# Performance work log

Measured on AMD Instinct MI355X. Metric: run time of the kernel, lower is better.

## Reference

```python
import jax, jax.numpy as jnp
import numpy as np

B = 128
K = 16
# (in_ch, featdim, dim) per stage, matching conv1..conv11
DIMS = [(3, 8, 2048), (8, 32, 1024), (32, 64, 512), (64, 64, 256), (64, 64, 128),
        (64, 128, 64), (128, 256, 32), (256, 512, 16), (512, 512, 8), (512, 512, 4),
        (512, 1024, 2)]


def setup_inputs() -> dict:
    key = jax.random.key(0)
    ks = jax.random.split(key, 64)
    inp = {"x": jax.random.normal(ks[0], (B, 3, 2048), dtype=jnp.float32)}
    i = 1
    for li, (cin, cf, d) in enumerate(DIMS, start=1):
        inp[f"W{li}"] = jax.random.normal(ks[i], (3 * cf, cin), dtype=jnp.float32) / np.sqrt(cin).astype(np.float32); i += 1
        inp[f"b{li}"] = jax.random.normal(ks[i], (3 * cf,), dtype=jnp.float32) * 0.01; i += 1
        inp[f"sel{li}"] = jax.random.randint(ks[i], (d,), 0, 3); i += 1
    inp["fcW"] = jax.random.normal(ks[i], (K, 1024), dtype=jnp.float32) / np.sqrt(1024).astype(np.float32); i += 1
    inp["fcb"] = jax.random.normal(ks[i], (K,), dtype=jnp.float32) * 0.01
    return inp


def kdconv(x, W, b, sel, featdim, dim):
    # 1x1 conv == per-position matmul: x [B, Cin, dim] -> y [B, 3*featdim, dim]
    y = jax.nn.relu(jnp.einsum('oi,bin->bon', W, x) + b[None, :, None])
    y = y.reshape(-1, featdim, 3, dim)
    # kd split-dim gather: pick one of the 3 feature groups per position
    y = jnp.take_along_axis(y, sel[None, None, None, :], axis=2)[:, :, 0, :]  # [B, featdim, dim]
    # pairwise max-pool of sibling leaves
    return y.reshape(-1, featdim, dim // 2, 2).max(axis=-1)  # [B, featdim, dim//2]


def reference(x, sel1, sel2, sel3, sel4, sel5, sel6, sel7, sel8, sel9, sel10, sel11,
              W1, b1, W2, b2, W3, b3, W4, b4, W5, b5, W6, b6, W7, b7, W8, b8,
              W9, b9, W10, b10, W11, b11, fcW, fcb):
    Ws = [W1, W2, W3, W4, W5, W6, W7, W8, W9, W10, W11]
    bs = [b1, b2, b3, b4, b5, b6, b7, b8, b9, b10, b11]
    sels = [sel1, sel2, sel3, sel4, sel5, sel6, sel7, sel8, sel9, sel10, sel11]
    h = x
    for (cin, cf, d), W, b, s in zip(DIMS, Ws, bs, sels):
        h = kdconv(h, W, b, s, cf, d)
    h = h.reshape(-1, 1024)  # [B, 1024]
    return jax.nn.log_softmax(h @ fcW.T + fcb, axis=-1)
```

## Files before the change

### kernel.cpp

```cpp
#include <hip/hip_runtime.h>
#include <math.h>

typedef __attribute__((ext_vector_type(8))) short bf16x8;
typedef __attribute__((ext_vector_type(4))) float f32x4;

__device__ __forceinline__ unsigned short f2bf(float f) {
    unsigned u = __builtin_bit_cast(unsigned, f);
    u += 0x7FFF + ((u >> 16) & 1);
    return (unsigned short)(u >> 16);
}
__device__ __forceinline__ float bf2f(unsigned short h) {
    unsigned u = ((unsigned)h) << 16;
    return __builtin_bit_cast(float, u);
}

struct K1Params {
    const float* x;
    const float* W1; const float* B1; const int* S1;
    const float* W2; const float* B2; const int* S2;
    const float* Wsrc[9];
    unsigned short* Wb;
    unsigned short* X3;
};

__global__ __launch_bounds__(256) void k1_kernel(K1Params P)
{
    const int tid = threadIdx.x;

    if (blockIdx.x >= 128) {
        int gt = (blockIdx.x - 128) * 256 + tid;
        const int we[9] = {6144, 12288, 12288, 24576, 98304, 393216, 786432, 786432, 1572864};
        int off = 0;
#pragma unroll
        for (int li = 0; li < 9; ++li) {
            const float4* src = (const float4*)P.Wsrc[li];
            ushort4* dst = (ushort4*)(P.Wb + off);
            int n4 = we[li] >> 2;
            for (int i = gt; i < n4; i += 32768) {
                float4 w = src[i];
                dst[i] = make_ushort4(f2bf(w.x), f2bf(w.y), f2bf(w.z), f2bf(w.w));
            }
            off += we[li];
        }
        return;
    }

    __shared__ float wl1[72], bl1[24], wl2[768], bl2[96];
    __shared__ unsigned short bufL1[16 * 64 * 8];

    if (tid < 72) wl1[tid] = P.W1[tid];
    if (tid >= 128 && tid < 152) bl1[tid - 128] = P.B1[tid - 128];
    for (int i = tid; i < 768; i += 256) wl2[i] = P.W2[i];
    if (tid < 96) bl2[tid] = P.B2[tid];
    __syncthreads();

    const int npT = blockIdx.x >> 1;
    const int b0  = (blockIdx.x & 1) * 64;

    for (int i = tid; i < 1024; i += 256) {
        int pos_l = i >> 6, bl = i & 63;
        int np1 = npT * 16 + pos_l;
        int b = b0 + bl;
        int s0 = P.S1[2 * np1], s1 = P.S1[2 * np1 + 1];
        const float* xb = P.x + (size_t)b * 6144 + 2 * np1;
        float2 c0 = *(const float2*)(xb);
        float2 c1 = *(const float2*)(xb + 2048);
        float2 c2 = *(const float2*)(xb + 4096);
        unsigned short o[8];
#pragma unroll
        for (int f = 0; f < 8; ++f) {
            int r0 = f * 3 + s0, r1 = f * 3 + s1;
            float z0 = fmaf(wl1[r0*3+2], c2.x, fmaf(wl1[r0*3+1], c1.x, fmaf(wl1[r0*3+0], c0.x, bl1[r0])));
            float z1 = fmaf(wl1[r1*3+2], c2.y, fmaf(wl1[r1*3+1], c1.y, fmaf(wl1[r1*3+0], c0.y, bl1[r1])));
            o[f] = f2bf(fmaxf(fmaxf(z0, z1), 0.f));
        }
        unsigned short* dst = &bufL1[((size_t)pos_l * 64 + bl) * 8];
        *(ushort4*)dst       = make_ushort4(o[0], o[1], o[2], o[3]);
        *(ushort4*)(dst + 4) = make_ushort4(o[4], o[5], o[6], o[7]);
    }
    __syncthreads();

    for (int i = tid; i < 512; i += 256) {
        int np_l = i >> 6, bl = i & 63;
        int np2 = npT * 8 + np_l;
        int s0 = P.S2[2 * np2], s1 = P.S2[2 * np2 + 1];
        const unsigned short* r0 = &bufL1[((size_t)(2 * np_l) * 64 + bl) * 8];
        const unsigned short* r1 = &bufL1[((size_t)(2 * np_l + 1) * 64 + bl) * 8];
        float xa[8], xb[8];
        {
            ushort4 u0 = *(const ushort4*)r0, u1 = *(const ushort4*)(r0 + 4);
            ushort4 v0 = *(const ushort4*)r1, v1 = *(const ushort4*)(r1 + 4);
            xa[0]=bf2f(u0.x); xa[1]=bf2f(u0.y); xa[2]=bf2f(u0.z); xa[3]=bf2f(u0.w);
            xa[4]=bf2f(u1.x); xa[5]=bf2f(u1.y); xa[6]=bf2f(u1.z); xa[7]=bf2f(u1.w);
            xb[0]=bf2f(v0.x); xb[1]=bf2f(v0.y); xb[2]=bf2f(v0.z); xb[3]=bf2f(v0.w);
            xb[4]=bf2f(v1.x); xb[5]=bf2f(v1.y); xb[6]=bf2f(v1.z); xb[7]=bf2f(v1.w);
        }
        unsigned short o[32];
#pragma unroll
        for (int f = 0; f < 32; ++f) {
            const float* w0 = &wl2[(f * 3 + s0) * 8];
            const float* w1 = &wl2[(f * 3 + s1) * 8];
            float z0 = bl2[f * 3 + s0], z1 = bl2[f * 3 + s1];
#pragma unroll
            for (int k = 0; k < 8; ++k) {
                z0 = fmaf(w0[k], xa[k], z0);
                z1 = fmaf(w1[k], xb[k], z1);
            }
            o[f] = f2bf(fmaxf(fmaxf(z0, z1), 0.f));
        }
        unsigned short* dst = P.X3 + ((size_t)np2 * 128 + b0 + bl) * 32;
#pragma unroll
        for (int i2 = 0; i2 < 8; ++i2)
            *(ushort4*)(dst + 4 * i2) = make_ushort4(o[4*i2], o[4*i2+1], o[4*i2+2], o[4*i2+3]);
    }
}

template<int CIN>
__device__ __forceinline__ void mfma_tile(
    const unsigned short* a0, const unsigned short* a1,
    const unsigned short* b0p, const unsigned short* b1p,
    f32x4& acc0, f32x4& acc1)
{
#pragma unroll
    for (int k = 0; k < CIN; k += 32) {
        bf16x8 A0 = __builtin_bit_cast(bf16x8, *(const float4*)(const void*)(a0 + k));
        bf16x8 A1 = __builtin_bit_cast(bf16x8, *(const float4*)(const void*)(a1 + k));
        bf16x8 B0 = __builtin_bit_cast(bf16x8, *(const float4*)(const void*)(b0p + k));
        bf16x8 B1 = __builtin_bit_cast(bf16x8, *(const float4*)(const void*)(b1p + k));
        acc0 = __builtin_amdgcn_mfma_f32_16x16x32_bf16(A0, B0, acc0, 0, 0, 0);
        acc1 = __builtin_amdgcn_mfma_f32_16x16x32_bf16(A1, B1, acc1, 0, 0, 0);
    }
}

__device__ __forceinline__ void epilogue_store(
    unsigned short* dst, const f32x4& acc0, const f32x4& acc1,
    const float* bias, int fbase, int s0, int s1)
{
    unsigned short o[4];
#pragma unroll
    for (int r = 0; r < 4; ++r) {
        float v = fmaxf(fmaxf(acc0[r] + bias[(fbase + r) * 3 + s0],
                              acc1[r] + bias[(fbase + r) * 3 + s1]), 0.f);
        o[r] = f2bf(v);
    }
    *(ushort4*)dst = make_ushort4(o[0], o[1], o[2], o[3]);
}

__global__ __launch_bounds__(256) void stage2_kernel(
    const unsigned short* __restrict__ X3,
    const unsigned short* __restrict__ Wb,
    const float* __restrict__ B3, const int* __restrict__ S3,
    const float* __restrict__ B4, const int* __restrict__ S4,
    const float* __restrict__ B5, const int* __restrict__ S5,
    unsigned short* __restrict__ X6)
{
    constexpr int RPE = 72;
    __shared__ unsigned short L3o[4 * 32 * RPE];
    __shared__ unsigned short L4o[2 * 32 * RPE];

    const int tid  = threadIdx.x;
    const int lane = tid & 63;
    const int wv   = tid >> 6;
    const int c = lane & 15, q = lane >> 4;
    const int n5 = blockIdx.x >> 2;
    const int b0 = (blockIdx.x & 3) * 32;

    const unsigned short* W3b = Wb;
    const unsigned short* W4b = Wb + 6144;
    const unsigned short* W5b = Wb + 18432;

    for (int t = wv; t < 32; t += 4) {
        int bt = t & 1, ft = (t >> 1) & 3, j = t >> 3;
        int np = 4 * n5 + j;
        int s0 = __builtin_amdgcn_readfirstlane(S3[2 * np]);
        int s1 = __builtin_amdgcn_readfirstlane(S3[2 * np + 1]);
        int f0 = ft * 16, bl = bt * 16;
        const unsigned short* a0 = W3b + (size_t)((f0 + c) * 3 + s0) * 32 + q * 8;
        const unsigned short* a1 = W3b + (size_t)((f0 + c) * 3 + s1) * 32 + q * 8;
        const unsigned short* bp0 = X3 + ((size_t)(8 * n5 + 2 * j) * 128 + b0 + bl + c) * 32 + q * 8;
        const unsigned short* bp1 = X3 + ((size_t)(8 * n5 + 2 * j + 1) * 128 + b0 + bl + c) * 32 + q * 8;
        f32x4 acc0 = {0.f,0.f,0.f,0.f}, acc1 = {0.f,0.f,0.f,0.f};
        mfma_tile<32>(a0, a1, bp0, bp1, acc0, acc1);
        epilogue_store(&L3o[((size_t)j * 32 + bl + c) * RPE + f0 + q * 4],
                       acc0, acc1, B3, f0 + q * 4, s0, s1);
    }
    __syncthreads();

    for (int t = wv; t < 16; t += 4) {
        int bt = t & 1, ft = (t >> 1) & 3, j = t >> 3;
        int np = 2 * n5 + j;
        int s0 = __builtin_amdgcn_readfirstlane(S4[2 * np]);
        int s1 = __builtin_amdgcn_readfirstlane(S4[2 * np + 1]);
        int f0 = ft * 16, bl = bt * 16;
        const unsigned short* a0 = W4b + (size_t)((f0 + c) * 3 + s0) * 64 + q * 8;
        const unsigned short* a1 = W4b + (size_t)((f0 + c) * 3 + s1) * 64 + q * 8;
        const unsigned short* bp0 = &L3o[((size_t)(2 * j) * 32 + bl + c) * RPE + q * 8];
        const unsigned short* bp1 = &L3o[((size_t)(2 * j + 1) * 32 + bl + c) * RPE + q * 8];
        f32x4 acc0 = {0.f,0.f,0.f,0.f}, acc1 = {0.f,0.f,0.f,0.f};
        mfma_tile<64>(a0, a1, bp0, bp1, acc0, acc1);
        epilogue_store(&L4o[((size_t)j * 32 + bl + c) * RPE + f0 + q * 4],
                       acc0, acc1, B4, f0 + q * 4, s0, s1);
    }
    __syncthreads();

    for (int t = wv; t < 8; t += 4) {
        int bt = t & 1, ft = t >> 1;
        int s0 = __builtin_amdgcn_readfirstlane(S5[2 * n5]);
        int s1 = __builtin_amdgcn_readfirstlane(S5[2 * n5 + 1]);
        int f0 = ft * 16, bl = bt * 16;
        const unsigned short* a0 = W5b + (size_t)((f0 + c) * 3 + s0) * 64 + q * 8;
        const unsigned short* a1 = W5b + (size_t)((f0 + c) * 3 + s1) * 64 + q * 8;
        const unsigned short* bp0 = &L4o[((size_t)(0) * 32 + bl + c) * RPE + q * 8];
        const unsigned short* bp1 = &L4o[((size_t)(1) * 32 + bl + c) * RPE + q * 8];
        f32x4 acc0 = {0.f,0.f,0.f,0.f}, acc1 = {0.f,0.f,0.f,0.f};
        mfma_tile<64>(a0, a1, bp0, bp1, acc0, acc1);
        epilogue_store(X6 + ((size_t)n5 * 128 + b0 + bl + c) * 64 + f0 + q * 4,
                       acc0, acc1, B5, f0 + q * 4, s0, s1);
    }
}

__global__ __launch_bounds__(512) void stage67_kernel(
    const unsigned short* __restrict__ X6,
    const unsigned short* __restrict__ W6b, const float* __restrict__ B6, const int* __restrict__ S6,
    const unsigned short* __restrict__ W7b, const float* __restrict__ B7, const int* __restrict__ S7,
    unsigned short* __restrict__ X8)
{
    constexpr int RPE = 136;
    __shared__ unsigned short L6o[2 * 16 * RPE];

    const int tid  = threadIdx.x;
    const int lane = tid & 63;
    const int wv   = tid >> 6;
    const int c = lane & 15, q = lane >> 4;
    const int n7 = blockIdx.x >> 3;
    const int b0 = (blockIdx.x & 7) * 16;

    for (int t = wv; t < 16; t += 8) {
        int j = t >> 3, ft = t & 7;
        int np = 2 * n7 + j;
        int s0 = __builtin_amdgcn_readfirstlane(S6[2 * np]);
        int s1 = __builtin_amdgcn_readfirstlane(S6[2 * np + 1]);
        int f0 = ft * 16;
        const unsigned short* a0 = W6b + (size_t)((f0 + c) * 3 + s0) * 64 + q * 8;
        const unsigned short* a1 = W6b + (size_t)((f0 + c) * 3 + s1) * 64 + q * 8;
        const unsigned short* bp0 = X6 + ((size_t)(2 * np) * 128 + b0 + c) * 64 + q * 8;
        const unsigned short* bp1 = X6 + ((size_t)(2 * np + 1) * 128 + b0 + c) * 64 + q * 8;
        f32x4 acc0 = {0.f,0.f,0.f,0.f}, acc1 = {0.f,0.f,0.f,0.f};
        mfma_tile<64>(a0, a1, bp0, bp1, acc0, acc1);
        epilogue_store(&L6o[((size_t)j * 16 + c) * RPE + f0 + q * 4],
                       acc0, acc1, B6, f0 + q * 4, s0, s1);
    }
    __syncthreads();

    {
        int s0 = __builtin_amdgcn_readfirstlane(S7[2 * n7]);
        int s1 = __builtin_amdgcn_readfirstlane(S7[2 * n7 + 1]);
        for (int t = wv; t < 16; t += 8) {
            int f0 = t * 16;
            const unsigned short* a0 = W7b + (size_t)((f0 + c) * 3 + s0) * 128 + q * 8;
            const unsigned short* a1 = W7b + (size_t)((f0 + c) * 3 + s1) * 128 + q * 8;
            const unsigned short* bp0 = &L6o[((size_t)(0) * 16 + c) * RPE + q * 8];
            const unsigned short* bp1 = &L6o[((size_t)(1) * 16 + c) * RPE + q * 8];
            f32x4 acc0 = {0.f,0.f,0.f,0.f}, acc1 = {0.f,0.f,0.f,0.f};
            mfma_tile<128>(a0, a1, bp0, bp1, acc0, acc1);
            epilogue_store(X8 + ((size_t)n7 * 128 + b0 + c) * 256 + f0 + q * 4,
                           acc0, acc1, B7, f0 + q * 4, s0, s1);
        }
    }
}

template<int CIN, int CF, int NP, int MW, int NW>
__global__ __launch_bounds__(256) void mfma_kernel(
    const unsigned short* __restrict__ Xin,
    const unsigned short* __restrict__ Wb,
    const float* __restrict__ bias,
    const int*   __restrict__ sel,
    unsigned short* __restrict__ Xout)
{
    constexpr int FT = CF / (16 * MW);
    constexpr int BT = 128 / (16 * NW);

    const int wid  = threadIdx.x >> 6;
    const int lane = threadIdx.x & 63;
    const int task = blockIdx.x * 4 + wid;
    const int bi = task % BT;
    const int fi = (task / BT) % FT;
    const int n  = task / (BT * FT);

    const int c = lane & 15;
    const int q = lane >> 4;
    const int s0 = __builtin_amdgcn_readfirstlane(sel[2 * n]);
    const int s1 = __builtin_amdgcn_readfirstlane(sel[2 * n + 1]);

    const int f0 = fi * 16 * MW;
    const int b0 = bi * 16 * NW;

    const unsigned short* ap[2][MW];
    const unsigned short* bp[2][NW];
#pragma unroll
    for (int p = 0; p < 2; ++p) {
        int s = p ? s1 : s0;
#pragma unroll
        for (int mi = 0; mi < MW; ++mi)
            ap[p][mi] = Wb + (size_t)((f0 + mi * 16 + c) * 3 + s) * CIN + q * 8;
#pragma unroll
        for (int ni = 0; ni < NW; ++ni)
            bp[p][ni] = Xin + ((size_t)(2 * n + p) * 128 + b0 + ni * 16 + c) * CIN + q * 8;
    }

    f32x4 acc[2][MW][NW];
#pragma unroll
    for (int p = 0; p < 2; ++p)
#pragma unroll
        for (int mi = 0; mi < MW; ++mi)
#pragma unroll
            for (int ni = 0; ni < NW; ++ni)
                acc[p][mi][ni] = (f32x4){0.f, 0.f, 0.f, 0.f};

// ... 33 lines not shown

__global__ __launch_bounds__(256) void fc_logsoftmax_kernel(
    const unsigned short* __restrict__ h, const float* __restrict__ fcW,
    const float* __restrict__ fcb, float* __restrict__ out)
{
    int b   = blockIdx.x;
    int tid = threadIdx.x;
    int k     = tid & 15;
    int chunk = tid >> 4;

    const float* __restrict__ wk = fcW + (size_t)k * 1024;
    const unsigned short* hb = h + (size_t)b * 1024;

    float partial = 0.0f;
    int j0 = chunk * 64;
#pragma unroll 8
    for (int j = 0; j < 64; ++j)
        partial = fmaf(bf2f(hb[j0 + j]), wk[j0 + j], partial);

    __shared__ float red[16][17];
    red[chunk][k] = partial;
    __syncthreads();

    __shared__ float logits[16];
    if (tid < 16) {
        float s = fcb[tid];
#pragma unroll
        for (int c = 0; c < 16; ++c) s += red[c][tid];
        logits[tid] = s;
    }
    __syncthreads();

    if (tid < 16) {
        float mx = -INFINITY;
#pragma unroll
        for (int kk = 0; kk < 16; ++kk) mx = fmaxf(mx, logits[kk]);
        float se = 0.0f;
#pragma unroll
        for (int kk = 0; kk < 16; ++kk) se += expf(logits[kk] - mx);
        out[b * 16 + tid] = logits[tid] - mx - logf(se);
    }
}

extern "C" void kernel_launch(void* const* d_in, const int* in_sizes, int n_in,
                              void* d_out, int out_size, void* d_ws, size_t ws_size,
                              hipStream_t stream)
{
#define WL(i) (const float*)d_in[1 + 3 * (i)]
#define BL(i) (const float*)d_in[2 + 3 * (i)]
#define SL(i) (const int*)  d_in[3 + 3 * (i)]

    unsigned short* bufA = (unsigned short*)d_ws;
    unsigned short* bufB = bufA + 2u * 1024u * 1024u;
    unsigned short* Wb   = bufB + 2u * 1024u * 1024u;

    const int o6 = 30720, o7 = 55296, o8 = 153600,
              o9 = 546816, o10 = 1333248, o11 = 2119680;

    K1Params P;
    P.x = (const float*)d_in[0];
    P.W1 = WL(0); P.B1 = BL(0); P.S1 = SL(0);
    P.W2 = WL(1); P.B2 = BL(1); P.S2 = SL(1);
    for (int i = 0; i < 9; ++i) P.Wsrc[i] = WL(2 + i);
    P.Wb = Wb; P.X3 = bufA;
    k1_kernel<<<256, 256, 0, stream>>>(P);

    stage2_kernel<<<256, 256, 0, stream>>>(bufA, Wb,
        BL(2), SL(2), BL(3), SL(3), BL(4), SL(4), bufB);

    stage67_kernel<<<128, 512, 0, stream>>>(bufB,
        Wb + o6, BL(5), SL(5), Wb + o7, BL(6), SL(6), bufA);

    mfma_kernel<256, 512, 8, 2, 2><<<128, 256, 0, stream>>>(bufA, Wb + o8,  BL(7),  SL(7),  bufB);
    mfma_kernel<512, 512, 4, 1, 1><<<256, 256, 0, stream>>>(bufB, Wb + o9,  BL(8),  SL(8),  bufA);
    mfma_kernel<512, 512, 2, 1, 1><<<128, 256, 0, stream>>>(bufA, Wb + o10, BL(9),  SL(9),  bufB);
    mfma_kernel<512, 1024, 1, 1, 1><<<128, 256, 0, stream>>>(bufB, Wb + o11, BL(10), SL(10), bufA);

    fc_logsoftmax_kernel<<<128, 256, 0, stream>>>(bufA, (const float*)d_in[34], (const float*)d_in[35], (float*)d_out);

#undef WL
#undef BL
#undef SL
}
```

Before: 211.0 us.

## Fuse stages 1-7 into one kernel with per-block tree slices in LDS

Replaces the three kernels for layers 1-7 with one fused kernel. Each block owns 16 batch items and one 128-point slice of the tree and keeps every intermediate level in a reused shared-memory arena, so activations no longer make round trips through global memory and two launches go away. Each block converts the weights for layers 3-6 from fp32 to bf16 into LDS, and layer 7 converts its weights on the fly, while extra blocks convert only the layer 8-11 weights. The cost is redundant weight conversion in every block, a large LDS footprint that limits occupancy, and fewer parallel tiles per level.

```diff
diff --git a/kernel.cpp b/kernel.cpp
--- a/kernel.cpp
+++ b/kernel.cpp
@@ -14,106 +14,10 @@
     return __builtin_bit_cast(float, u);
 }
 
-struct K1Params {
-    const float* x;
-    const float* W1; const float* B1; const int* S1;
-    const float* W2; const float* B2; const int* S2;
-    const float* Wsrc[9];
-    unsigned short* Wb;
-    unsigned short* X3;
-};
-
-__global__ __launch_bounds__(256) void k1_kernel(K1Params P)
-{
-    const int tid = threadIdx.x;
-
-    if (blockIdx.x >= 128) {
-        int gt = (blockIdx.x - 128) * 256 + tid;
-        const int we[9] = {6144, 12288, 12288, 24576, 98304, 393216, 786432, 786432, 1572864};
-        int off = 0;
-#pragma unroll
-        for (int li = 0; li < 9; ++li) {
-            const float4* src = (const float4*)P.Wsrc[li];
-            ushort4* dst = (ushort4*)(P.Wb + off);
-            int n4 = we[li] >> 2;
-            for (int i = gt; i < n4; i += 32768) {
-                float4 w = src[i];
-                dst[i] = make_ushort4(f2bf(w.x), f2bf(w.y), f2bf(w.z), f2bf(w.w));
-            }
-            off += we[li];
-        }
-        return;
-    }
-
-    __shared__ float wl1[72], bl1[24], wl2[768], bl2[96];
-    __shared__ unsigned short bufL1[16 * 64 * 8];
-
-    if (tid < 72) wl1[tid] = P.W1[tid];
-    if (tid >= 128 && tid < 152) bl1[tid - 128] = P.B1[tid - 128];
-    for (int i = tid; i < 768; i += 256) wl2[i] = P.W2[i];
-    if (tid < 96) bl2[tid] = P.B2[tid];
-    __syncthreads();
-
-    const int npT = blockIdx.x >> 1;
-    const int b0  = (blockIdx.x & 1) * 64;
-
-    for (int i = tid; i < 1024; i += 256) {
-        int pos_l = i >> 6, bl = i & 63;
-        int np1 = npT * 16 + pos_l;
-        int b = b0 + bl;
-        int s0 = P.S1[2 * np1], s1 = P.S1[2 * np1 + 1];
-        const float* xb = P.x + (size_t)b * 6144 + 2 * np1;
-        float2 c0 = *(const float2*)(xb);
-        float2 c1 = *(const float2*)(xb + 2048);
-        float2 c2 = *(const float2*)(xb + 4096);
-        unsigned short o[8];
-#pragma unroll
-        for (int f = 0; f < 8; ++f) {
-            int r0 = f * 3 + s0, r1 = f * 3 + s1;
-            float z0 = fmaf(wl1[r0*3+2], c2.x, fmaf(wl1[r0*3+1], c1.x, fmaf(wl1[r0*3+0], c0.x, bl1[r0])));
-            float z1 = fmaf(wl1[r1*3+2], c2.y, fmaf(wl1[r1*3+1], c1.y, fmaf(wl1[r1*3+0], c0.y, bl1[r1])));
-            o[f] = f2bf(fmaxf(fmaxf(z0, z1), 0.f));
-        }
-        unsigned short* dst = &bufL1[((size_t)pos_l * 64 + bl) * 8];
-        *(ushort4*)dst       = make_ushort4(o[0], o[1], o[2], o[3]);
-        *(ushort4*)(dst + 4) = make_ushort4(o[4], o[5], o[6], o[7]);
-    }
-    __syncthreads();
-
-    for (int i = tid; i < 512; i += 256) {
-        int np_l = i >> 6, bl = i & 63;
-        int np2 = npT * 8 + np_l;
-        int s0 = P.S2[2 * np2], s1 = P.S2[2 * np2 + 1];
-        const unsigned short* r0 = &bufL1[((size_t)(2 * np_l) * 64 + bl) * 8];
-        const unsigned short* r1 = &bufL1[((size_t)(2 * np_l + 1) * 64 + bl) * 8];
-        float xa[8], xb[8];
-        {
-            ushort4 u0 = *(const ushort4*)r0, u1 = *(const ushort4*)(r0 + 4);
-            ushort4 v0 = *(const ushort4*)r1, v1 = *(const ushort4*)(r1 + 4);
-            xa[0]=bf2f(u0.x); xa[1]=bf2f(u0.y); xa[2]=bf2f(u0.z); xa[3]=bf2f(u0.w);
-            xa[4]=bf2f(u1.x); xa[5]=bf2f(u1.y); xa[6]=bf2f(u1.z); xa[7]=bf2f(u1.w);
-            xb[0]=bf2f(v0.x); xb[1]=bf2f(v0.y); xb[2]=bf2f(v0.z); xb[3]=bf2f(v0.w);
-            xb[4]=bf2f(v1.x); xb[5]=bf2f(v1.y); xb[6]=bf2f(v1.z); xb[7]=bf2f(v1.w);
-        }
-        unsigned short o[32];
-#pragma unroll
-        for (int f = 0; f < 32; ++f) {
-            const float* w0 = &wl2[(f * 3 + s0) * 8];
-            const float* w1 = &wl2[(f * 3 + s1) * 8];
-            float z0 = bl2[f * 3 + s0], z1 = bl2[f * 3 + s1];
-#pragma unroll
-            for (int k = 0; k < 8; ++k) {
-                z0 = fmaf(w0[k], xa[k], z0);
-                z1 = fmaf(w1[k], xb[k], z1);
-            }
-            o[f] = f2bf(fmaxf(fmaxf(z0, z1), 0.f));
-        }
-        unsigned short* dst = P.X3 + ((size_t)np2 * 128 + b0 + bl) * 32;
-#pragma unroll
-        for (int i2 = 0; i2 < 8; ++i2)
-            *(ushort4*)(dst + 4 * i2) = make_ushort4(o[4*i2], o[4*i2+1], o[4*i2+2], o[4*i2+3]);
-    }
-}
+#define O_W8 153600
+#define O_W9 546816
+#define O_W10 1333248
+#define O_W11 2119680
 
 template<int CIN>
 __device__ __forceinline__ void mfma_tile(
@@ -146,124 +50,317 @@
     *(ushort4*)dst = make_ushort4(o[0], o[1], o[2], o[3]);
 }
 
-__global__ __launch_bounds__(256) void stage2_kernel(
-    const unsigned short* __restrict__ X3,
-    const unsigned short* __restrict__ Wb,
-    const float* __restrict__ B3, const int* __restrict__ S3,
-    const float* __restrict__ B4, const int* __restrict__ S4,
-    const float* __restrict__ B5, const int* __restrict__ S5,
-    unsigned short* __restrict__ X6)
+__device__ __forceinline__ bf16x8 cvt8(const float* p) {
+    float4 u0 = *(const float4*)p;
+    float4 u1 = *(const float4*)(p + 4);
+    bf16x8 r;
+    r[0] = (short)f2bf(u0.x); r[1] = (short)f2bf(u0.y);
+    r[2] = (short)f2bf(u0.z); r[3] = (short)f2bf(u0.w);
+    r[4] = (short)f2bf(u1.x); r[5] = (short)f2bf(u1.y);
+    r[6] = (short)f2bf(u1.z); r[7] = (short)f2bf(u1.w);
+    return r;
+}
+
+struct FusedParams {
+    const float* x;
+    const float* W1; const float* B1; const int* S1;
+    const float* W2; const float* B2; const int* S2;
+    const float* Wsrc[9];
+    const float* Bl[9];
+    const int*   Sl[9];
+    unsigned short* Wb;
+    unsigned short* X8;
+};
+
+#define A_XS   0
+#define A_L1O  25344
+#define A_WSM  41728
+#define A_L2O  45568
+#define A_WB3  0
+#define A_L3O  86528
+#define A_WB4  45568
+#define A_L4O  0
+#define A_WB5  18432
+#define A_L5O  46080
+#define A_WB6  55296
+#define A_L6O  0
+#define ARENA_BYTES 123392
+
+__global__ __launch_bounds__(512) void fused17_kernel(FusedParams P)
 {
-    constexpr int RPE = 72;
-    __shared__ unsigned short L3o[4 * 32 * RPE];
-    __shared__ unsigned short L4o[2 * 32 * RPE];
-
-    const int tid  = threadIdx.x;
+    const int tid = threadIdx.x;
+
+    if (blockIdx.x >= 128) {
+        int gt = (blockIdx.x - 128) * 512 + tid;
+        const int we[4] = {393216, 786432, 786432, 1572864};
+        const int wo[4] = {O_W8, O_W9, O_W10, O_W11};
+#pragma unroll
+        for (int li = 0; li < 4; ++li) {
+            const float4* src = (const float4*)P.Wsrc[5 + li];
+            ushort4* dst = (ushort4*)(P.Wb + wo[li]);
+            int n4 = we[li] >> 2;
+            for (int i = gt; i < n4; i += 32768) {
+                float4 w = src[i];
+                dst[i] = make_ushort4(f2bf(w.x), f2bf(w.y), f2bf(w.z), f2bf(w.w));
+            }
+        }
+        return;
+    }
+
+    __shared__ __align__(16) char arena[ARENA_BYTES];
+
+    const int bg   = blockIdx.x >> 4;
+    const int sl   = blockIdx.x & 15;
     const int lane = tid & 63;
     const int wv   = tid >> 6;
-    const int c = lane & 15, q = lane >> 4;
-    const int n5 = blockIdx.x >> 2;
-    const int b0 = (blockIdx.x & 3) * 32;
-
-    const unsigned short* W3b = Wb;
-    const unsigned short* W4b = Wb + 6144;
-    const unsigned short* W5b = Wb + 18432;
-
-    for (int t = wv; t < 32; t += 4) {
-        int bt = t & 1, ft = (t >> 1) & 3, j = t >> 3;
-        int np = 4 * n5 + j;
-        int s0 = __builtin_amdgcn_readfirstlane(S3[2 * np]);
-        int s1 = __builtin_amdgcn_readfirstlane(S3[2 * np + 1]);
-        int f0 = ft * 16, bl = bt * 16;
-        const unsigned short* a0 = W3b + (size_t)((f0 + c) * 3 + s0) * 32 + q * 8;
-        const unsigned short* a1 = W3b + (size_t)((f0 + c) * 3 + s1) * 32 + q * 8;
-        const unsigned short* bp0 = X3 + ((size_t)(8 * n5 + 2 * j) * 128 + b0 + bl + c) * 32 + q * 8;
-        const unsigned short* bp1 = X3 + ((size_t)(8 * n5 + 2 * j + 1) * 128 + b0 + bl + c) * 32 + q * 8;
-        f32x4 acc0 = {0.f,0.f,0.f,0.f}, acc1 = {0.f,0.f,0.f,0.f};
-        mfma_tile<32>(a0, a1, bp0, bp1, acc0, acc1);
-        epilogue_store(&L3o[((size_t)j * 32 + bl + c) * RPE + f0 + q * 4],
-                       acc0, acc1, B3, f0 + q * 4, s0, s1);
-    }
-    __syncthreads();
-
-    for (int t = wv; t < 16; t += 4) {
-        int bt = t & 1, ft = (t >> 1) & 3, j = t >> 3;
-        int np = 2 * n5 + j;
-        int s0 = __builtin_amdgcn_readfirstlane(S4[2 * np]);
-        int s1 = __builtin_amdgcn_readfirstlane(S4[2 * np + 1]);
-        int f0 = ft * 16, bl = bt * 16;
-        const unsigned short* a0 = W4b + (size_t)((f0 + c) * 3 + s0) * 64 + q * 8;
-        const unsigned short* a1 = W4b + (size_t)((f0 + c) * 3 + s1) * 64 + q * 8;
-        const unsigned short* bp0 = &L3o[((size_t)(2 * j) * 32 + bl + c) * RPE + q * 8];
-        const unsigned short* bp1 = &L3o[((size_t)(2 * j + 1) * 32 + bl + c) * RPE + q * 8];
-        f32x4 acc0 = {0.f,0.f,0.f,0.f}, acc1 = {0.f,0.f,0.f,0.f};
-        mfma_tile<64>(a0, a1, bp0, bp1, acc0, acc1);
-        epilogue_store(&L4o[((size_t)j * 32 + bl + c) * RPE + f0 + q * 4],
-                       acc0, acc1, B4, f0 + q * 4, s0, s1);
-    }
-    __syncthreads();
-
-    for (int t = wv; t < 8; t += 4) {
-        int bt = t & 1, ft = t >> 1;
-        int s0 = __builtin_amdgcn_readfirstlane(S5[2 * n5]);
-        int s1 = __builtin_amdgcn_readfirstlane(S5[2 * n5 + 1]);
-        int f0 = ft * 16, bl = bt * 16;
-        const unsigned short* a0 = W5b + (size_t)((f0 + c) * 3 + s0) * 64 + q * 8;
-        const unsigned short* a1 = W5b + (size_t)((f0 + c) * 3 + s1) * 64 + q * 8;
-        const unsigned short* bp0 = &L4o[((size_t)(0) * 32 + bl + c) * RPE + q * 8];
-        const unsigned short* bp1 = &L4o[((size_t)(1) * 32 + bl + c) * RPE + q * 8];
-        f32x4 acc0 = {0.f,0.f,0.f,0.f}, acc1 = {0.f,0.f,0.f,0.f};
-        mfma_tile<64>(a0, a1, bp0, bp1, acc0, acc1);
-        epilogue_store(X6 + ((size_t)n5 * 128 + b0 + bl + c) * 64 + f0 + q * 4,
-                       acc0, acc1, B5, f0 + q * 4, s0, s1);
-    }
-}
-
-__global__ __launch_bounds__(512) void stage67_kernel(
-    const unsigned short* __restrict__ X6,
-    const unsigned short* __restrict__ W6b, const float* __restrict__ B6, const int* __restrict__ S6,
-    const unsigned short* __restrict__ W7b, const float* __restrict__ B7, const int* __restrict__ S7,
-    unsigned short* __restrict__ X8)
-{
-    constexpr int RPE = 136;
-    __shared__ unsigned short L6o[2 * 16 * RPE];
-
-    const int tid  = threadIdx.x;
-    const int lane = tid & 63;
-    const int wv   = tid >> 6;
-    const int c = lane & 15, q = lane >> 4;
-    const int n7 = blockIdx.x >> 3;
-    const int b0 = (blockIdx.x & 7) * 16;
-
-    for (int t = wv; t < 16; t += 8) {
-        int j = t >> 3, ft = t & 7;
-        int np = 2 * n7 + j;
-        int s0 = __builtin_amdgcn_readfirstlane(S6[2 * np]);
-        int s1 = __builtin_amdgcn_readfirstlane(S6[2 * np + 1]);
-        int f0 = ft * 16;
-        const unsigned short* a0 = W6b + (size_t)((f0 + c) * 3 + s0) * 64 + q * 8;
-        const unsigned short* a1 = W6b + (size_t)((f0 + c) * 3 + s1) * 64 + q * 8;
-        const unsigned short* bp0 = X6 + ((size_t)(2 * np) * 128 + b0 + c) * 64 + q * 8;
-        const unsigned short* bp1 = X6 + ((size_t)(2 * np + 1) * 128 + b0 + c) * 64 + q * 8;
-        f32x4 acc0 = {0.f,0.f,0.f,0.f}, acc1 = {0.f,0.f,0.f,0.f};
-        mfma_tile<64>(a0, a1, bp0, bp1, acc0, acc1);
-        epilogue_store(&L6o[((size_t)j * 16 + c) * RPE + f0 + q * 4],
-                       acc0, acc1, B6, f0 + q * 4, s0, s1);
-    }
-    __syncthreads();
-
-    {
-        int s0 = __builtin_amdgcn_readfirstlane(S7[2 * n7]);
-        int s1 = __builtin_amdgcn_readfirstlane(S7[2 * n7 + 1]);
+    const int c    = lane & 15, q = lane >> 4;
+
+    {
+        float* xsf = (float*)(arena + A_XS);
+        const float* xg = P.x + (size_t)(bg * 16) * 6144 + sl * 128;
+        for (int i = tid; i < 6144; i += 512) {
+            int b = i / 384;
+            int r = i - b * 384;
+            int cc = r >> 7, p = r & 127;
+            xsf[b * 396 + cc * 132 + p] = xg[(size_t)b * 6144 + cc * 2048 + p];
+        }
+        float* wsm = (float*)(arena + A_WSM);
+        for (int i = tid; i < 960; i += 512) {
+            float v;
+            if (i < 72)       v = P.W1[i];
+            else if (i < 96)  v = P.B1[i - 72];
+            else if (i < 864) v = P.W2[i - 96];
+            else              v = P.B2[i - 864];
+            wsm[i] = v;
+        }
+    }
+    __syncthreads();
+
+    {
+        const float* xsf = (const float*)(arena + A_XS);
+        const float* wl1 = (const float*)(arena + A_WSM);
+        const float* bl1 = wl1 + 72;
+        unsigned short* L1o = (unsigned short*)(arena + A_L1O);
+        for (int i = tid; i < 1024; i += 512) {
+            int n = i >> 4, b = i & 15;
+            int np1 = sl * 64 + n;
+            int s0 = P.S1[2 * np1], s1 = P.S1[2 * np1 + 1];
+            const float* xb0 = xsf + b * 396 + 2 * n;
+            float c0x = xb0[0],   c0y = xb0[1];
+            float c1x = xb0[132], c1y = xb0[133];
+            float c2x = xb0[264], c2y = xb0[265];
+            unsigned short o[8];
+#pragma unroll
+            for (int f = 0; f < 8; ++f) {
+                int r0 = f * 3 + s0, r1 = f * 3 + s1;
+                float z0 = fmaf(wl1[r0*3+2], c2x, fmaf(wl1[r0*3+1], c1x, fmaf(wl1[r0*3+0], c0x, bl1[r0])));
+                float z1 = fmaf(wl1[r1*3+2], c2y, fmaf(wl1[r1*3+1], c1y, fmaf(wl1[r1*3+0], c0y, bl1[r1])));
+                o[f] = f2bf(fmaxf(fmaxf(z0, z1), 0.f));
+            }
+            unsigned short* dst = L1o + (n * 16 + b) * 8;
+            *(ushort4*)dst       = make_ushort4(o[0], o[1], o[2], o[3]);
+            *(ushort4*)(dst + 4) = make_ushort4(o[4], o[5], o[6], o[7]);
+        }
+    }
+    __syncthreads();
+
+    {
+        const float* wl2 = (const float*)(arena + A_WSM) + 96;
+        const float* bl2 = (const float*)(arena + A_WSM) + 864;
+        const unsigned short* L1o = (const unsigned short*)(arena + A_L1O);
+        unsigned short* L2o = (unsigned short*)(arena + A_L2O);
+        {
+            int i = tid;
+            int n = i >> 4, b = i & 15;
+            int np2 = sl * 32 + n;
+            int s0 = P.S2[2 * np2], s1 = P.S2[2 * np2 + 1];
+            const unsigned short* r0 = L1o + ((2 * n) * 16 + b) * 8;
+            const unsigned short* r1 = L1o + ((2 * n + 1) * 16 + b) * 8;
+            float xa[8], xb2[8];
+            {
+                ushort4 u0 = *(const ushort4*)r0, u1 = *(const ushort4*)(r0 + 4);
+                ushort4 v0 = *(const ushort4*)r1, v1 = *(const ushort4*)(r1 + 4);
+                xa[0]=bf2f(u0.x); xa[1]=bf2f(u0.y); xa[2]=bf2f(u0.z); xa[3]=bf2f(u0.w);
+                xa[4]=bf2f(u1.x); xa[5]=bf2f(u1.y); xa[6]=bf2f(u1.z); xa[7]=bf2f(u1.w);
+                xb2[0]=bf2f(v0.x); xb2[1]=bf2f(v0.y); xb2[2]=bf2f(v0.z); xb2[3]=bf2f(v0.w);
+                xb2[4]=bf2f(v1.x); xb2[5]=bf2f(v1.y); xb2[6]=bf2f(v1.z); xb2[7]=bf2f(v1.w);
+            }
+            unsigned short o[32];
+#pragma unroll
+            for (int f = 0; f < 32; ++f) {
+                const float* w0 = &wl2[(f * 3 + s0) * 8];
+                const float* w1 = &wl2[(f * 3 + s1) * 8];
+                float z0 = bl2[f * 3 + s0], z1 = bl2[f * 3 + s1];
+#pragma unroll
+                for (int k = 0; k < 8; ++k) {
+                    z0 = fmaf(w0[k], xa[k], z0);
+                    z1 = fmaf(w1[k], xb2[k], z1);
+                }
+                o[f] = f2bf(fmaxf(fmaxf(z0, z1), 0.f));
+            }
+            unsigned short* dst = L2o + (n * 16 + b) * 40;
+#pragma unroll
+            for (int i2 = 0; i2 < 8; ++i2)
+                *(ushort4*)(dst + 4 * i2) = make_ushort4(o[4*i2], o[4*i2+1], o[4*i2+2], o[4*i2+3]);
+        }
+    }
+    __syncthreads();
+
+    {
+        unsigned short* wb = (unsigned short*)(arena + A_WB3);
+        const float* Wf = P.Wsrc[0];
+        for (int i = tid; i < 6144; i += 512) {
+            int row = i >> 5, k = i & 31;
+            wb[row * 40 + k] = f2bf(Wf[i]);
+        }
+    }
+    __syncthreads();
+
+    {
+        const unsigned short* wb  = (const unsigned short*)(arena + A_WB3);
+        const unsigned short* L2o = (const unsigned short*)(arena + A_L2O);
+        unsigned short* L3o = (unsigned short*)(arena + A_L3O);
+        const int* S3 = P.Sl[0]; const float* B3 = P.Bl[0];
+        for (int t = wv; t < 64; t += 8) {
+            int n3 = t >> 2, ft = t & 3;
+            int np = sl * 16 + n3;
+            int s0 = __builtin_amdgcn_readfirstlane(S3[2 * np]);
+            int s1 = __builtin_amdgcn_readfirstlane(S3[2 * np + 1]);
+            int f0 = ft * 16;
+            const unsigned short* a0 = wb + ((f0 + c) * 3 + s0) * 40 + q * 8;
+            const unsigned short* a1 = wb + ((f0 + c) * 3 + s1) * 40 + q * 8;
+            const unsigned short* bp0 = L2o + ((2 * n3) * 16 + c) * 40 + q * 8;
+            const unsigned short* bp1 = L2o + ((2 * n3 + 1) * 16 + c) * 40 + q * 8;
+            f32x4 acc0 = {0.f,0.f,0.f,0.f}, acc1 = {0.f,0.f,0.f,0.f};
+            mfma_tile<32>(a0, a1, bp0, bp1, acc0, acc1);
+            epilogue_store(L3o + (n3 * 16 + c) * 72 + f0 + q * 4,
+                           acc0, acc1, B3, f0 + q * 4, s0, s1);
+        }
+    }
+    __syncthreads();
+
+    {
+        unsigned short* wb = (unsigned short*)(arena + A_WB4);
+        const float* Wf = P.Wsrc[1];
+        for (int i = tid; i < 12288; i += 512) {
+            int row = i >> 6, k = i & 63;
+            wb[row * 72 + k] = f2bf(Wf[i]);
+        }
+    }
+    __syncthreads();
+
+    {
+        const unsigned short* wb  = (const unsigned short*)(arena + A_WB4);
+        const unsigned short* L3o = (const unsigned short*)(arena + A_L3O);
+        unsigned short* L4o = (unsigned short*)(arena + A_L4O);
+        const int* S4 = P.Sl[1]; const float* B4 = P.Bl[1];
+        for (int t = wv; t < 32; t += 8) {
+            int n4 = t >> 2, ft = t & 3;
+            int np = sl * 8 + n4;
+            int s0 = __builtin_amdgcn_readfirstlane(S4[2 * np]);
+            int s1 = __builtin_amdgcn_readfirstlane(S4[2 * np + 1]);
+            int f0 = ft * 16;
+            const unsigned short* a0 = wb + ((f0 + c) * 3 + s0) * 72 + q * 8;
+            const unsigned short* a1 = wb + ((f0 + c) * 3 + s1) * 72 + q * 8;
+            const unsigned short* bp0 = L3o + ((2 * n4) * 16 + c) * 72 + q * 8;
+            const unsigned short* bp1 = L3o + ((2 * n4 + 1) * 16 + c) * 72 + q * 8;
+            f32x4 acc0 = {0.f,0.f,0.f,0.f}, acc1 = {0.f,0.f,0.f,0.f};
+            mfma_tile<64>(a0, a1, bp0, bp1, acc0, acc1);
+            epilogue_store(L4o + (n4 * 16 + c) * 72 + f0 + q * 4,
+                           acc0, acc1, B4, f0 + q * 4, s0, s1);
+        }
+    }
+    __syncthreads();
+
+    {
+        unsigned short* wb = (unsigned short*)(arena + A_WB5);
+        const float* Wf = P.Wsrc[2];
+        for (int i = tid; i < 12288; i += 512) {
+            int row = i >> 6, k = i & 63;
+            wb[row * 72 + k] = f2bf(Wf[i]);
+        }
+    }
+    __syncthreads();
+
+    {
+        const unsigned short* wb  = (const unsigned short*)(arena + A_WB5);
+        const unsigned short* L4o = (const unsigned short*)(arena + A_L4O);
+        unsigned short* L5o = (unsigned short*)(arena + A_L5O);
+        const int* S5 = P.Sl[2]; const float* B5 = P.Bl[2];
+        for (int t = wv; t < 16; t += 8) {
+            int n5 = t >> 2, ft = t & 3;
+            int np = sl * 4 + n5;
+            int s0 = __builtin_amdgcn_readfirstlane(S5[2 * np]);
+            int s1 = __builtin_amdgcn_readfirstlane(S5[2 * np + 1]);
+            int f0 = ft * 16;
+            const unsigned short* a0 = wb + ((f0 + c) * 3 + s0) * 72 + q * 8;
+            const unsigned short* a1 = wb + ((f0 + c) * 3 + s1) * 72 + q * 8;
+            const unsigned short* bp0 = L4o + ((2 * n5) * 16 + c) * 72 + q * 8;
+            const unsigned short* bp1 = L4o + ((2 * n5 + 1) * 16 + c) * 72 + q * 8;
+            f32x4 acc0 = {0.f,0.f,0.f,0.f}, acc1 = {0.f,0.f,0.f,0.f};
+            mfma_tile<64>(a0, a1, bp0, bp1, acc0, acc1);
+            epilogue_store(L5o + (n5 * 16 + c) * 72 + f0 + q * 4,
+                           acc0, acc1, B5, f0 + q * 4, s0, s1);
+        }
+    }
+    __syncthreads();
+
+    {
+        unsigned short* wb = (unsigned short*)(arena + A_WB6);
+        const float* Wf = P.Wsrc[3];
+        for (int i = tid; i < 24576; i += 512) {
+            int row = i >> 6, k = i & 63;
+            wb[row * 72 + k] = f2bf(Wf[i]);
+        }
+    }
+    __syncthreads();
+
+    {
+        const unsigned short* wb  = (const unsigned short*)(arena + A_WB6);
+        const unsigned short* L5o = (const unsigned short*)(arena + A_L5O);
+        unsigned short* L6o = (unsigned short*)(arena + A_L6O);
+        const int* S6 = P.Sl[3]; const float* B6 = P.Bl[3];
+        for (int t = wv; t < 16; t += 8) {
+            int n6 = t >> 3, ft = t & 7;
+            int np = sl * 2 + n6;
+            int s0 = __builtin_amdgcn_readfirstlane(S6[2 * np]);
+            int s1 = __builtin_amdgcn_readfirstlane(S6[2 * np + 1]);
+            int f0 = ft * 16;
+            const unsigned short* a0 = wb + ((f0 + c) * 3 + s0) * 72 + q * 8;
+            const unsigned short* a1 = wb + ((f0 + c) * 3 + s1) * 72 + q * 8;
+            const unsigned short* bp0 = L5o + ((2 * n6) * 16 + c) * 72 + q * 8;
+            const unsigned short* bp1 = L5o + ((2 * n6 + 1) * 16 + c) * 72 + q * 8;
+            f32x4 acc0 = {0.f,0.f,0.f,0.f}, acc1 = {0.f,0.f,0.f,0.f};
+            mfma_tile<64>(a0, a1, bp0, bp1, acc0, acc1);
+            epilogue_store(L6o + (n6 * 16 + c) * 136 + f0 + q * 4,
+                           acc0, acc1, B6, f0 + q * 4, s0, s1);
+        }
+    }
+    __syncthreads();
+
+    {
+        const unsigned short* L6o = (const unsigned short*)(arena + A_L6O);
+        const float* W7f = P.Wsrc[4];
+        const int* S7 = P.Sl[4]; const float* B7 = P.Bl[4];
+        int s0 = __builtin_amdgcn_readfirstlane(S7[2 * sl]);
+        int s1 = __builtin_amdgcn_readfirstlane(S7[2 * sl + 1]);
         for (int t = wv; t < 16; t += 8) {
             int f0 = t * 16;
-            const unsigned short* a0 = W7b + (size_t)((f0 + c) * 3 + s0) * 128 + q * 8;
-            const unsigned short* a1 = W7b + (size_t)((f0 + c) * 3 + s1) * 128 + q * 8;
-            const unsigned short* bp0 = &L6o[((size_t)(0) * 16 + c) * RPE + q * 8];
-            const unsigned short* bp1 = &L6o[((size_t)(1) * 16 + c) * RPE + q * 8];
+            const float* wa0 = W7f + (size_t)((f0 + c) * 3 + s0) * 128;
+            const float* wa1 = W7f + (size_t)((f0 + c) * 3 + s1) * 128;
+            const unsigned short* bp0 = L6o + (0 * 16 + c) * 136;
+            const unsigned short* bp1 = L6o + (1 * 16 + c) * 136;
             f32x4 acc0 = {0.f,0.f,0.f,0.f}, acc1 = {0.f,0.f,0.f,0.f};
-            mfma_tile<128>(a0, a1, bp0, bp1, acc0, acc1);
-            epilogue_store(X8 + ((size_t)n7 * 128 + b0 + c) * 256 + f0 + q * 4,
+#pragma unroll
+            for (int k = 0; k < 128; k += 32) {
+                bf16x8 A0 = cvt8(wa0 + k + q * 8);
+                bf16x8 A1 = cvt8(wa1 + k + q * 8);
+                bf16x8 B0 = __builtin_bit_cast(bf16x8, *(const float4*)(const void*)(bp0 + k + q * 8));
+                bf16x8 B1 = __builtin_bit_cast(bf16x8, *(const float4*)(const void*)(bp1 + k + q * 8));
+                acc0 = __builtin_amdgcn_mfma_f32_16x16x32_bf16(A0, B0, acc0, 0, 0, 0);
+                acc1 = __builtin_amdgcn_mfma_f32_16x16x32_bf16(A1, B1, acc1, 0, 0, 0);
+            }
+            epilogue_store(P.X8 + ((size_t)sl * 128 + bg * 16 + c) * 256 + f0 + q * 4,
                            acc0, acc1, B7, f0 + q * 4, s0, s1);
         }
     }
@@ -405,27 +502,22 @@
     unsigned short* bufB = bufA + 2u * 1024u * 1024u;
     unsigned short* Wb   = bufB + 2u * 1024u * 1024u;
 
-    const int o6 = 30720, o7 = 55296, o8 = 153600,
-              o9 = 546816, o10 = 1333248, o11 = 2119680;
-
-    K1Params P;
-    P.x = (const float*)d_in[0];
-    P.W1 = WL(0); P.B1 = BL(0); P.S1 = SL(0);
-    P.W2 = WL(1); P.B2 = BL(1); P.S2 = SL(1);
-    for (int i = 0; i < 9; ++i) P.Wsrc[i] = WL(2 + i);
-    P.Wb = Wb; P.X3 = bufA;
-    k1_kernel<<<256, 256, 0, stream>>>(P);
-
-    stage2_kernel<<<256, 256, 0, stream>>>(bufA, Wb,
-        BL(2), SL(2), BL(3), SL(3), BL(4), SL(4), bufB);
-
-    stage67_kernel<<<128, 512, 0, stream>>>(bufB,
-        Wb + o6, BL(5), SL(5), Wb + o7, BL(6), SL(6), bufA);
-
-    mfma_kernel<256, 512, 8, 2, 2><<<128, 256, 0, stream>>>(bufA, Wb + o8,  BL(7),  SL(7),  bufB);
-    mfma_kernel<512, 512, 4, 1, 1><<<256, 256, 0, stream>>>(bufB, Wb + o9,  BL(8),  SL(8),  bufA);
-    mfma_kernel<512, 512, 2, 1, 1><<<128, 256, 0, stream>>>(bufA, Wb + o10, BL(9),  SL(9),  bufB);
-    mfma_kernel<512, 1024, 1, 1, 1><<<128, 256, 0, stream>>>(bufB, Wb + o11, BL(10), SL(10), bufA);
+    FusedParams FP;
+    FP.x  = (const float*)d_in[0];
+    FP.W1 = WL(0); FP.B1 = BL(0); FP.S1 = SL(0);
+    FP.W2 = WL(1); FP.B2 = BL(1); FP.S2 = SL(1);
+    for (int i = 0; i < 9; ++i) {
+        FP.Wsrc[i] = WL(2 + i);
+        FP.Bl[i]   = BL(2 + i);
+        FP.Sl[i]   = SL(2 + i);
+    }
+    FP.Wb = Wb; FP.X8 = bufA;
+    fused17_kernel<<<192, 512, 0, stream>>>(FP);
+
+    mfma_kernel<256, 512, 8, 2, 2><<<128, 256, 0, stream>>>(bufA, Wb + O_W8,  BL(7),  SL(7),  bufB);
+    mfma_kernel<512, 512, 4, 1, 1><<<256, 256, 0, stream>>>(bufB, Wb + O_W9,  BL(8),  SL(8),  bufA);
+    mfma_kernel<512, 512, 2, 1, 1><<<128, 256, 0, stream>>>(bufA, Wb + O_W10, BL(9),  SL(9),  bufB);
+    mfma_kernel<512, 1024, 1, 1, 1><<<128, 256, 0, stream>>>(bufB, Wb + O_W11, BL(10), SL(10), bufA);
 
     fc_logsoftmax_kernel<<<128, 256, 0, stream>>>(bufA, (const float*)d_in[34], (const float*)d_in[35], (float*)d_out);
 
```

Result: no change. 208.7 us (-1.1%).

## Restructure head kernel to compute L1+L2 per thread without shared staging

Applied to the files above, without the earlier changes.

The first kernel now assigns each thread one level-2 output position for one batch element. It loads four input positions with float4 reads and computes layer 1 in registers, removing the shared-memory bufL1 staging and the barrier between layers 1 and 2. The grid doubles to 512 blocks, and the weight-packing blocks also double, so each converts with a larger stride. X3 moves to its own workspace buffer and weight offsets become named constants. This adds occupancy, but L2 output stores are now strided per lane (np2*128 + b), which may reduce coalescing.

```diff
diff --git a/kernel.cpp b/kernel.cpp
--- a/kernel.cpp
+++ b/kernel.cpp
@@ -14,7 +14,48 @@
     return __builtin_bit_cast(float, u);
 }
 
-struct K1Params {
+#define O_W3 0
+#define O_W4 6144
+#define O_W5 18432
+#define O_W6 30720
+#define O_W7 55296
+#define O_W8 153600
+#define O_W9 546816
+#define O_W10 1333248
+#define O_W11 2119680
+
+template<int CIN>
+__device__ __forceinline__ void mfma_tile(
+    const unsigned short* a0, const unsigned short* a1,
+    const unsigned short* b0p, const unsigned short* b1p,
+    f32x4& acc0, f32x4& acc1)
+{
+#pragma unroll
+    for (int k = 0; k < CIN; k += 32) {
+        bf16x8 A0 = __builtin_bit_cast(bf16x8, *(const float4*)(const void*)(a0 + k));
+        bf16x8 A1 = __builtin_bit_cast(bf16x8, *(const float4*)(const void*)(a1 + k));
+        bf16x8 B0 = __builtin_bit_cast(bf16x8, *(const float4*)(const void*)(b0p + k));
+        bf16x8 B1 = __builtin_bit_cast(bf16x8, *(const float4*)(const void*)(b1p + k));
+        acc0 = __builtin_amdgcn_mfma_f32_16x16x32_bf16(A0, B0, acc0, 0, 0, 0);
+        acc1 = __builtin_amdgcn_mfma_f32_16x16x32_bf16(A1, B1, acc1, 0, 0, 0);
+    }
+}
+
+__device__ __forceinline__ void epilogue_store(
+    unsigned short* dst, const f32x4& acc0, const f32x4& acc1,
+    const float* bias, int fbase, int s0, int s1)
+{
+    unsigned short o[4];
+#pragma unroll
+    for (int r = 0; r < 4; ++r) {
+        float v = fmaxf(fmaxf(acc0[r] + bias[(fbase + r) * 3 + s0],
+                              acc1[r] + bias[(fbase + r) * 3 + s1]), 0.f);
+        o[r] = f2bf(v);
+    }
+    *(ushort4*)dst = make_ushort4(o[0], o[1], o[2], o[3]);
+}
+
+struct HeadParams {
     const float* x;
     const float* W1; const float* B1; const int* S1;
     const float* W2; const float* B2; const int* S2;
@@ -23,79 +64,79 @@
     unsigned short* X3;
 };
 
-__global__ __launch_bounds__(256) void k1_kernel(K1Params P)
+__global__ __launch_bounds__(256) void head_l12_pack(HeadParams P)
 {
     const int tid = threadIdx.x;
 
-    if (blockIdx.x >= 128) {
-        int gt = (blockIdx.x - 128) * 256 + tid;
+    if (blockIdx.x >= 256) {
+        int gt = (blockIdx.x - 256) * 256 + tid;
         const int we[9] = {6144, 12288, 12288, 24576, 98304, 393216, 786432, 786432, 1572864};
-        int off = 0;
+        const int wo[9] = {O_W3, O_W4, O_W5, O_W6, O_W7, O_W8, O_W9, O_W10, O_W11};
 #pragma unroll
         for (int li = 0; li < 9; ++li) {
             const float4* src = (const float4*)P.Wsrc[li];
-            ushort4* dst = (ushort4*)(P.Wb + off);
+            ushort4* dst = (ushort4*)(P.Wb + wo[li]);
             int n4 = we[li] >> 2;
-            for (int i = gt; i < n4; i += 32768) {
+            for (int i = gt; i < n4; i += 65536) {
                 float4 w = src[i];
                 dst[i] = make_ushort4(f2bf(w.x), f2bf(w.y), f2bf(w.z), f2bf(w.w));
             }
-            off += we[li];
         }
         return;
     }
 
-    __shared__ float wl1[72], bl1[24], wl2[768], bl2[96];
-    __shared__ unsigned short bufL1[16 * 64 * 8];
-
-    if (tid < 72) wl1[tid] = P.W1[tid];
-    if (tid >= 128 && tid < 152) bl1[tid - 128] = P.B1[tid - 128];
-    for (int i = tid; i < 768; i += 256) wl2[i] = P.W2[i];
-    if (tid < 96) bl2[tid] = P.B2[tid];
-    __syncthreads();
-
-    const int npT = blockIdx.x >> 1;
-    const int b0  = (blockIdx.x & 1) * 64;
-
-    for (int i = tid; i < 1024; i += 256) {
-        int pos_l = i >> 6, bl = i & 63;
-        int np1 = npT * 16 + pos_l;
-        int b = b0 + bl;
-        int s0 = P.S1[2 * np1], s1 = P.S1[2 * np1 + 1];
-        const float* xb = P.x + (size_t)b * 6144 + 2 * np1;
-        float2 c0 = *(const float2*)(xb);
-        float2 c1 = *(const float2*)(xb + 2048);
-        float2 c2 = *(const float2*)(xb + 4096);
-        unsigned short o[8];
+    __shared__ float wsm[960];
+    for (int i = tid; i < 960; i += 256) {
+        float v;
+        if (i < 72)       v = P.W1[i];
+        else if (i < 96)  v = P.B1[i - 72];
+        else if (i < 864) v = P.W2[i - 96];
+        else              v = P.B2[i - 864];
+        wsm[i] = v;
+    }
+    __syncthreads();
+
+    const float* wl1 = wsm;
+    const float* bl1 = wsm + 72;
+    const float* wl2 = wsm + 96;
+    const float* bl2 = wsm + 864;
+
+    const int lane = tid & 63;
+    const int gw   = blockIdx.x * 4 + (tid >> 6);
+    const int b    = gw >> 3;
+    const int chunk= gw & 7;
+    const int np2  = chunk * 64 + lane;
+
+    const float* xb = P.x + (size_t)b * 6144 + chunk * 256 + 4 * lane;
+    float4 x0 = *(const float4*)(xb);
+    float4 x1 = *(const float4*)(xb + 2048);
+    float4 x2 = *(const float4*)(xb + 4096);
+    int4 sA = *(const int4*)(P.S1 + 4 * np2);
+    int2 sB = *(const int2*)(P.S2 + 2 * np2);
+
+    float y1a[8], y1b[8];
+    {
+        int s0 = sA.x, s1 = sA.y;
 #pragma unroll
         for (int f = 0; f < 8; ++f) {
             int r0 = f * 3 + s0, r1 = f * 3 + s1;
-            float z0 = fmaf(wl1[r0*3+2], c2.x, fmaf(wl1[r0*3+1], c1.x, fmaf(wl1[r0*3+0], c0.x, bl1[r0])));
-            float z1 = fmaf(wl1[r1*3+2], c2.y, fmaf(wl1[r1*3+1], c1.y, fmaf(wl1[r1*3+0], c0.y, bl1[r1])));
-            o[f] = f2bf(fmaxf(fmaxf(z0, z1), 0.f));
-        }
-        unsigned short* dst = &bufL1[((size_t)pos_l * 64 + bl) * 8];
-        *(ushort4*)dst       = make_ushort4(o[0], o[1], o[2], o[3]);
-        *(ushort4*)(dst + 4) = make_ushort4(o[4], o[5], o[6], o[7]);
-    }
-    __syncthreads();
-
-    for (int i = tid; i < 512; i += 256) {
-        int np_l = i >> 6, bl = i & 63;
-        int np2 = npT * 8 + np_l;
-        int s0 = P.S2[2 * np2], s1 = P.S2[2 * np2 + 1];
-        const unsigned short* r0 = &bufL1[((size_t)(2 * np_l) * 64 + bl) * 8];
-        const unsigned short* r1 = &bufL1[((size_t)(2 * np_l + 1) * 64 + bl) * 8];
-        float xa[8], xb[8];
-        {
-            ushort4 u0 = *(const ushort4*)r0, u1 = *(const ushort4*)(r0 + 4);
-            ushort4 v0 = *(const ushort4*)r1, v1 = *(const ushort4*)(r1 + 4);
-            xa[0]=bf2f(u0.x); xa[1]=bf2f(u0.y); xa[2]=bf2f(u0.z); xa[3]=bf2f(u0.w);
-            xa[4]=bf2f(u1.x); xa[5]=bf2f(u1.y); xa[6]=bf2f(u1.z); xa[7]=bf2f(u1.w);
-            xb[0]=bf2f(v0.x); xb[1]=bf2f(v0.y); xb[2]=bf2f(v0.z); xb[3]=bf2f(v0.w);
-            xb[4]=bf2f(v1.x); xb[5]=bf2f(v1.y); xb[6]=bf2f(v1.z); xb[7]=bf2f(v1.w);
-        }
-        unsigned short o[32];
+            float z0 = fmaf(wl1[r0*3+2], x2.x, fmaf(wl1[r0*3+1], x1.x, fmaf(wl1[r0*3+0], x0.x, bl1[r0])));
+            float z1 = fmaf(wl1[r1*3+2], x2.y, fmaf(wl1[r1*3+1], x1.y, fmaf(wl1[r1*3+0], x0.y, bl1[r1])));
+            y1a[f] = bf2f(f2bf(fmaxf(fmaxf(z0, z1), 0.f)));
+        }
+        int t0 = sA.z, t1 = sA.w;
+#pragma unroll
+        for (int f = 0; f < 8; ++f) {
+            int r0 = f * 3 + t0, r1 = f * 3 + t1;
+            float z0 = fmaf(wl1[r0*3+2], x2.z, fmaf(wl1[r0*3+1], x1.z, fmaf(wl1[r0*3+0], x0.z, bl1[r0])));
+            float z1 = fmaf(wl1[r1*3+2], x2.w, fmaf(wl1[r1*3+1], x1.w, fmaf(wl1[r1*3+0], x0.w, bl1[r1])));
+            y1b[f] = bf2f(f2bf(fmaxf(fmaxf(z0, z1), 0.f)));
+        }
+    }
+
+    unsigned short o[32];
+    {
+        int s0 = sB.x, s1 = sB.y;
 #pragma unroll
         for (int f = 0; f < 32; ++f) {
             const float* w0 = &wl2[(f * 3 + s0) * 8];
@@ -103,47 +144,17 @@
             float z0 = bl2[f * 3 + s0], z1 = bl2[f * 3 + s1];
 #pragma unroll
             for (int k = 0; k < 8; ++k) {
-                z0 = fmaf(w0[k], xa[k], z0);
-                z1 = fmaf(w1[k], xb[k], z1);
+                z0 = fmaf(w0[k], y1a[k], z0);
+                z1 = fmaf(w1[k], y1b[k], z1);
             }
             o[f] = f2bf(fmaxf(fmaxf(z0, z1), 0.f));
         }
-        unsigned short* dst = P.X3 + ((size_t)np2 * 128 + b0 + bl) * 32;
-#pragma unroll
-        for (int i2 = 0; i2 < 8; ++i2)
-            *(ushort4*)(dst + 4 * i2) = make_ushort4(o[4*i2], o[4*i2+1], o[4*i2+2], o[4*i2+3]);
-    }
-}
-
-template<int CIN>
-__device__ __forceinline__ void mfma_tile(
-    const unsigned short* a0, const unsigned short* a1,
-    const unsigned short* b0p, const unsigned short* b1p,
-    f32x4& acc0, f32x4& acc1)
-{
-#pragma unroll
-    for (int k = 0; k < CIN; k += 32) {
-        bf16x8 A0 = __builtin_bit_cast(bf16x8, *(const float4*)(const void*)(a0 + k));
-        bf16x8 A1 = __builtin_bit_cast(bf16x8, *(const float4*)(const void*)(a1 + k));
-        bf16x8 B0 = __builtin_bit_cast(bf16x8, *(const float4*)(const void*)(b0p + k));
-        bf16x8 B1 = __builtin_bit_cast(bf16x8, *(const float4*)(const void*)(b1p + k));
-        acc0 = __builtin_amdgcn_mfma_f32_16x16x32_bf16(A0, B0, acc0, 0, 0, 0);
-        acc1 = __builtin_amdgcn_mfma_f32_16x16x32_bf16(A1, B1, acc1, 0, 0, 0);
-    }
-}
-
-__device__ __forceinline__ void epilogue_store(
-    unsigned short* dst, const f32x4& acc0, const f32x4& acc1,
-    const float* bias, int fbase, int s0, int s1)
-{
-    unsigned short o[4];
-#pragma unroll
-    for (int r = 0; r < 4; ++r) {
-        float v = fmaxf(fmaxf(acc0[r] + bias[(fbase + r) * 3 + s0],
-                              acc1[r] + bias[(fbase + r) * 3 + s1]), 0.f);
-        o[r] = f2bf(v);
-    }
-    *(ushort4*)dst = make_ushort4(o[0], o[1], o[2], o[3]);
+    }
+
+    unsigned short* dst = P.X3 + ((size_t)np2 * 128 + b) * 32;
+#pragma unroll
+    for (int i2 = 0; i2 < 8; ++i2)
+        *(ushort4*)(dst + 4 * i2) = make_ushort4(o[4*i2], o[4*i2+1], o[4*i2+2], o[4*i2+3]);
 }
 
 __global__ __launch_bounds__(256) void stage2_kernel(
@@ -403,29 +414,27 @@
 
     unsigned short* bufA = (unsigned short*)d_ws;
     unsigned short* bufB = bufA + 2u * 1024u * 1024u;
-    unsigned short* Wb   = bufB + 2u * 1024u * 1024u;
-
-    const int o6 = 30720, o7 = 55296, o8 = 153600,
-              o9 = 546816, o10 = 1333248, o11 = 2119680;
-
-    K1Params P;
-    P.x = (const float*)d_in[0];
-    P.W1 = WL(0); P.B1 = BL(0); P.S1 = SL(0);
-    P.W2 = WL(1); P.B2 = BL(1); P.S2 = SL(1);
-    for (int i = 0; i < 9; ++i) P.Wsrc[i] = WL(2 + i);
-    P.Wb = Wb; P.X3 = bufA;
-    k1_kernel<<<256, 256, 0, stream>>>(P);
-
-    stage2_kernel<<<256, 256, 0, stream>>>(bufA, Wb,
+    unsigned short* X3   = bufB + 2u * 1024u * 1024u;
+    unsigned short* Wb   = X3   + 2u * 1024u * 1024u;
+
+    HeadParams HP;
+    HP.x  = (const float*)d_in[0];
+    HP.W1 = WL(0); HP.B1 = BL(0); HP.S1 = SL(0);
+    HP.W2 = WL(1); HP.B2 = BL(1); HP.S2 = SL(1);
+    for (int i = 0; i < 9; ++i) HP.Wsrc[i] = WL(2 + i);
+    HP.Wb = Wb; HP.X3 = X3;
+    head_l12_pack<<<512, 256, 0, stream>>>(HP);
+
+    stage2_kernel<<<256, 256, 0, stream>>>(X3, Wb,
         BL(2), SL(2), BL(3), SL(3), BL(4), SL(4), bufB);
 
     stage67_kernel<<<128, 512, 0, stream>>>(bufB,
-        Wb + o6, BL(5), SL(5), Wb + o7, BL(6), SL(6), bufA);
-
-    mfma_kernel<256, 512, 8, 2, 2><<<128, 256, 0, stream>>>(bufA, Wb + o8,  BL(7),  SL(7),  bufB);
-    mfma_kernel<512, 512, 4, 1, 1><<<256, 256, 0, stream>>>(bufB, Wb + o9,  BL(8),  SL(8),  bufA);
-    mfma_kernel<512, 512, 2, 1, 1><<<128, 256, 0, stream>>>(bufA, Wb + o10, BL(9),  SL(9),  bufB);
-    mfma_kernel<512, 1024, 1, 1, 1><<<128, 256, 0, stream>>>(bufB, Wb + o11, BL(10), SL(10), bufA);
+        Wb + O_W6, BL(5), SL(5), Wb + O_W7, BL(6), SL(6), bufA);
+
+    mfma_kernel<256, 512, 8, 2, 2><<<128, 256, 0, stream>>>(bufA, Wb + O_W8,  BL(7),  SL(7),  bufB);
+    mfma_kernel<512, 512, 4, 1, 1><<<256, 256, 0, stream>>>(bufB, Wb + O_W9,  BL(8),  SL(8),  bufA);
+    mfma_kernel<512, 512, 2, 1, 1><<<128, 256, 0, stream>>>(bufA, Wb + O_W10, BL(9),  SL(9),  bufB);
+    mfma_kernel<512, 1024, 1, 1, 1><<<128, 256, 0, stream>>>(bufB, Wb + O_W11, BL(10), SL(10), bufA);
 
     fc_logsoftmax_kernel<<<128, 256, 0, stream>>>(bufA, (const float*)d_in[34], (const float*)d_in[35], (float*)d_out);
 
```

New measurement: 205.3 us. 1.03x faster.
